# Kernel tuning notes

Hardware: AMD Instinct MI355X
Metric: run time of the kernel (lower is better)

The kernel has to match this reference:

```python
import jax, jax.numpy as jnp
import numpy as np

B, L, D = 4, 2048, 1024
H = 16
HD = D // H  # head_dim = 64
BASE = 10000.0


def rope_cos_sin(seq_len, head_dim, dtype=jnp.float32):
    inv_freq = 1.0 / (BASE ** (jnp.arange(0, head_dim, 2, dtype=jnp.float32) / head_dim))
    t = jnp.arange(seq_len, dtype=jnp.float32)
    freqs = jnp.outer(t, inv_freq)  # [L, HD/2]
    return jnp.cos(freqs).astype(dtype), jnp.sin(freqs).astype(dtype)


def apply_rope(x, cos, sin):
    # x: [B, H, L, HD]; cos/sin: [L, HD/2]
    x1 = x[..., ::2]
    x2 = x[..., 1::2]
    c = cos[None, None, :, :]
    s = sin[None, None, :, :]
    # NOTE: original concatenates halves (does not re-interleave)
    return jnp.concatenate([x1 * c - x2 * s, x1 * s + x2 * c], axis=-1)


def setup_inputs() -> dict:
    key = jax.random.key(0)
    k1, k2, k3 = jax.random.split(key, 3)
    x = jax.random.normal(k1, (B, L, D), dtype=jnp.float32)
    W_qkv = jax.random.normal(k2, (3 * D, D), dtype=jnp.float32) * (D ** -0.5)
    W_proj = jax.random.normal(k3, (D, D), dtype=jnp.float32) * (D ** -0.5)
    return {"x": x, "W_qkv": W_qkv, "W_proj": W_proj}


def reference(x, W_qkv, W_proj):
    b, l, d = x.shape
    scale = HD ** -0.5
    qkv = jnp.einsum('bld,ed->ble', x, W_qkv)            # [B, L, 3D]
    qkv = qkv.reshape(b, l, 3, H, HD)
    q, k, v = (jnp.transpose(qkv[:, :, i], (0, 2, 1, 3)) for i in range(3))  # [B,H,L,HD]
    cos, sin = rope_cos_sin(l, HD, x.dtype)
    q = apply_rope(q, cos, sin)
    k = apply_rope(k, cos, sin)
    attn = jnp.einsum('bhqd,bhkd->bhqk', q, k) * scale   # [B,H,L,L]
    attn = jax.nn.softmax(attn, axis=-1)
    out = jnp.einsum('bhqk,bhkd->bhqd', attn, v)         # [B,H,L,HD]
    out = jnp.transpose(out, (0, 2, 1, 3)).reshape(b, l, d)
    return jnp.einsum('bld,ed->ble', out, W_proj)
```

## Files before the change

kernel.cpp:

```cpp
#include <hip/hip_runtime.h>
#include <hip/hip_bf16.h>

typedef unsigned short u16;
typedef unsigned int u32;
typedef __attribute__((ext_vector_type(8))) short bf16x8;
typedef __attribute__((ext_vector_type(4))) float f32x4;

#define NL 2048
#define NH 16

__device__ __forceinline__ float bf2f(u16 v) {
    union { float f; unsigned u; } x; x.u = ((unsigned)v) << 16; return x.f;
}
__device__ __forceinline__ u16 f2bf(float f) {
    union { __hip_bfloat16 h; u16 u; } x; x.h = __float2bfloat16(f); return x.u;
}
__device__ __forceinline__ u32 pk2(float a, float b) {
    union { float f; u32 u; } x, y; x.f = a; y.f = b;
    return ((x.u + 0x8000u) >> 16) | ((y.u + 0x8000u) & 0xffff0000u);
}
__device__ __forceinline__ u32 pkt(float lo, float hi) {
    union { float f; u32 u; } x, y; x.f = lo; y.f = hi;
    return __builtin_amdgcn_perm(y.u, x.u, 0x07060302u);
}
#if __has_builtin(__builtin_amdgcn_exp2f)
#define EXP2F(x) __builtin_amdgcn_exp2f(x)
#else
#define EXP2F(x) __expf((x) * 0.69314718056f)
#endif

__device__ __forceinline__ void gload_lds16(const u16* g, u16* l) {
    __builtin_amdgcn_global_load_lds(
        (__attribute__((address_space(1))) void*)(g),
        (__attribute__((address_space(3))) void*)(l), 16, 0, 0);
}

__global__ __launch_bounds__(256) void cast_all_k(const float* __restrict__ x,
                                                  const float* __restrict__ wq,
                                                  const float* __restrict__ wp,
                                                  u16* __restrict__ xo,
                                                  u16* __restrict__ wqo,
                                                  u16* __restrict__ wpo) {
    int i = blockIdx.x * 256 + threadIdx.x;
    const float* src; u16* dst; int off;
    if (i < 2097152)      { src = x;  dst = xo;  off = i; }
    else if (i < 2883584) { src = wq; dst = wqo; off = i - 2097152; }
    else                  { src = wp; dst = wpo; off = i - 2883584; }
    float4 v = *(const float4*)&src[(size_t)off * 4];
    u16 tmp[4] = {f2bf(v.x), f2bf(v.y), f2bf(v.z), f2bf(v.w)};
    *(ushort4*)&dst[(size_t)off * 4] = *(ushort4*)tmp;
}

__global__ __launch_bounds__(256) void rope_table_k(float* __restrict__ cosT,
                                                    float* __restrict__ sinT) {
    int idx = blockIdx.x * 256 + threadIdx.x;
    int l = idx >> 5, i = idx & 31;
    float invf = exp2f(-(float)i * 0.41524101186092029f);
    float ang = (float)l * invf;
    cosT[idx] = cosf(ang);
    sinT[idx] = sinf(ang);
}

template <typename OutT>
__global__ __launch_bounds__(256) void gemm_bt(const u16* __restrict__ A,
                                               const u16* __restrict__ Bm,
                                               OutT* __restrict__ C,
                                               int M, int N, int K) {
    __shared__ u16 As[128][64];
    __shared__ u16 Bs[128][64];
    const int t = threadIdx.x;
    const int lane = t & 63, wave = t >> 6;
    const int quad = lane >> 4, lrow = lane & 15;
    const int wr = wave >> 1, wc = wave & 1;
    const size_t m0 = (size_t)blockIdx.y * 128, n0 = (size_t)blockIdx.x * 128;

    const int srow = wave * 32 + (lane >> 3);
    const int scg  = (lane & 7) ^ (lane >> 3);

    f32x4 acc[4][4];
#pragma unroll
    for (int i = 0; i < 4; ++i)
#pragma unroll
        for (int j = 0; j < 4; ++j) acc[i][j] = (f32x4)0.0f;

    for (int k0 = 0; k0 < K; k0 += 64) {
#pragma unroll
        for (int j = 0; j < 4; ++j) {
            gload_lds16(&A[(m0 + srow + j * 8) * K + k0 + scg * 8],
                        &As[wave * 32 + j * 8][0]);
            gload_lds16(&Bm[(n0 + srow + j * 8) * K + k0 + scg * 8],
                        &Bs[wave * 32 + j * 8][0]);
        }
        __syncthreads();
#pragma unroll
        for (int ks = 0; ks < 2; ++ks) {
            bf16x8 av[4], bv[4];
#pragma unroll
            for (int i = 0; i < 4; ++i)
                av[i] = *(const bf16x8*)
                    &As[wr * 64 + i * 16 + lrow][(((ks << 2) | quad) ^ (lrow & 7)) << 3];
#pragma unroll
            for (int j = 0; j < 4; ++j)
                bv[j] = *(const bf16x8*)
                    &Bs[wc * 64 + j * 16 + lrow][(((ks << 2) | quad) ^ (lrow & 7)) << 3];
#pragma unroll
            for (int i = 0; i < 4; ++i)
#pragma unroll
                for (int j = 0; j < 4; ++j)
                    acc[i][j] = __builtin_amdgcn_mfma_f32_16x16x32_bf16(
                        av[i], bv[j], acc[i][j], 0, 0, 0);
        }
        __syncthreads();
    }
#pragma unroll
    for (int i = 0; i < 4; ++i)
#pragma unroll
        for (int r = 0; r < 4; ++r) {
            size_t row = m0 + wr * 64 + i * 16 + quad * 4 + r;
#pragma unroll
            for (int j = 0; j < 4; ++j) {
                size_t col = n0 + wc * 64 + j * 16 + lrow;
                if constexpr (sizeof(OutT) == 4)
                    C[row * N + col] = acc[i][j][r];
                else
                    C[row * N + col] = f2bf(acc[i][j][r]);
            }
        }
}

__global__ __launch_bounds__(256) void rope_vt_k(const u16* __restrict__ qkv,
                                                 const float* __restrict__ cosT,
                                                 const float* __restrict__ sinT,
                                                 u16* __restrict__ Q,
                                                 u16* __restrict__ Ko,
                                                 u16* __restrict__ VT) {
    __shared__ u16 vtile[64][72];
    const int lt = blockIdx.x, bh = blockIdx.y;
    const int b = bh >> 4, h = bh & 15;
    const int l0 = lt * 64;
    const int t = threadIdx.x;
    const float SC = 0.180336879f;
#pragma unroll
    for (int c = 0; c < 2; ++c) {
        int flat8 = c * 256 + t;
        int li = flat8 >> 3, dg = flat8 & 7;
        const u16* rowp = qkv + (size_t)(b * NL + l0 + li) * 3072 + h * 64 + dg * 8;
        uint4 qv = *(const uint4*)rowp;
        uint4 kv = *(const uint4*)(rowp + 1024);
        uint4 vv = *(const uint4*)(rowp + 2048);
        *(uint4*)&vtile[li][dg * 8] = vv;
        float4 cs = *(const float4*)&cosT[(l0 + li) * 32 + dg * 4];
        float4 sn = *(const float4*)&sinT[(l0 + li) * 32 + dg * 4];
        union { float f; u32 u; } w;
        float e0, o0, e1, o1, e2, o2, e3, o3;
        w.u = qv.x << 16; e0 = w.f; w.u = qv.x & 0xffff0000u; o0 = w.f;
        w.u = qv.y << 16; e1 = w.f; w.u = qv.y & 0xffff0000u; o1 = w.f;
        w.u = qv.z << 16; e2 = w.f; w.u = qv.z & 0xffff0000u; o2 = w.f;
        w.u = qv.w << 16; e3 = w.f; w.u = qv.w & 0xffff0000u; o3 = w.f;
        float c0 = cs.x * SC, c1 = cs.y * SC, c2 = cs.z * SC, c3 = cs.w * SC;
        float s0 = sn.x * SC, s1 = sn.y * SC, s2 = sn.z * SC, s3 = sn.w * SC;
        size_t ob = ((size_t)(b * NH + h) * NL + l0 + li) * 64;
        *(uint2*)&Q[ob + dg * 4] =
            make_uint2(pk2(e0 * c0 - o0 * s0, e1 * c1 - o1 * s1),
                       pk2(e2 * c2 - o2 * s2, e3 * c3 - o3 * s3));
        *(uint2*)&Q[ob + 32 + dg * 4] =
            make_uint2(pk2(e0 * s0 + o0 * c0, e1 * s1 + o1 * c1),
                       pk2(e2 * s2 + o2 * c2, e3 * s3 + o3 * c3));
        float f0, g0, f1, g1, f2, g2, f3, g3;
        w.u = kv.x << 16; f0 = w.f; w.u = kv.x & 0xffff0000u; g0 = w.f;
        w.u = kv.y << 16; f1 = w.f; w.u = kv.y & 0xffff0000u; g1 = w.f;
        w.u = kv.z << 16; f2 = w.f; w.u = kv.z & 0xffff0000u; g2 = w.f;
        w.u = kv.w << 16; f3 = w.f; w.u = kv.w & 0xffff0000u; g3 = w.f;
        *(uint2*)&Ko[ob + dg * 4] =
            make_uint2(pk2(f0 * cs.x - g0 * sn.x, f1 * cs.y - g1 * sn.y),
                       pk2(f2 * cs.z - g2 * sn.z, f3 * cs.w - g3 * sn.w));
        *(uint2*)&Ko[ob + 32 + dg * 4] =
            make_uint2(pk2(f0 * sn.x + g0 * cs.x, f1 * sn.y + g1 * cs.y),
                       pk2(f2 * sn.z + g2 * cs.z, f3 * sn.w + g3 * cs.w));
    }
    __syncthreads();
#pragma unroll
    for (int c = 0; c < 2; ++c) {
        int flat8 = c * 256 + t;
        int d = flat8 >> 3, lg = flat8 & 7;
        u16 tmp[8];
#pragma unroll
        for (int e = 0; e < 8; ++e) tmp[e] = vtile[lg * 8 + e][d];
        *(uint4*)&VT[((size_t)(bh * 64 + d)) * NL + l0 + lg * 8] = *(uint4*)tmp;
    }
}

__global__ __launch_bounds__(512, 4) void attn_k(const u16* __restrict__ Q,
                                                 const u16* __restrict__ Kg,
                                                 const u16* __restrict__ VT,
                                                 u16* __restrict__ Og) {
    __shared__ __align__(16) char smem[65536];
    u16 (*KsB)[64][64] = (u16(*)[64][64])(smem);
    u16 (*VsB)[64][64] = (u16(*)[64][64])(smem + 16384);
    u16* PsBase = (u16*)(smem + 32768);
    const int t = threadIdx.x;
    const int lane = t & 63, wave = t >> 6;
    const int quad = lane >> 4, lq = lane & 15;
    u16* PsW = PsBase + wave * 2048;

    const int qt = blockIdx.x, bh = blockIdx.y;
    const int q0 = qt * 256;
    const size_t qkbase = (size_t)bh * NL * 64;

    const int rsub = lane >> 3;
    const int scg  = (lane & 7) ^ rsub;

    u16 (*Qtmp)[64] = (u16(*)[64])(smem + 32768);
#pragma unroll
    for (int j = 0; j < 4; ++j)
        gload_lds16(&Q[qkbase + (size_t)(q0 + wave * 32 + j * 8 + rsub) * 64 + scg * 8],
                    &Qtmp[wave * 32 + j * 8][0]);
    const u16* kptr = Kg + qkbase + (size_t)(wave * 8 + rsub) * 64 + scg * 8;
    const u16* vptr = VT + qkbase + (size_t)(wave * 8 + rsub) * NL + scg * 8;
    gload_lds16(kptr, &KsB[0][wave * 8][0]);
    gload_lds16(vptr, &VsB[0][wave * 8][0]);
    kptr += 64 * 64;
    vptr += 64;
    __syncthreads();
    bf16x8 bq[2][2];
#pragma unroll
    for (int qh = 0; qh < 2; ++qh)
#pragma unroll
        for (int ks = 0; ks < 2; ++ks)
            bq[qh][ks] = *(const bf16x8*)
                &Qtmp[wave * 32 + qh * 16 + lq][(((ks << 2) | quad) ^ (lq & 7)) << 3];

    const bf16x8 ones = (bf16x8)(short)16256;
    f32x4 ot[2][4];
#pragma unroll
    for (int qh = 0; qh < 2; ++qh)
#pragma unroll
        for (int mt = 0; mt < 4; ++mt) ot[qh][mt] = (f32x4)0.0f;
    f32x4 lacc[2] = {(f32x4)0.0f, (f32x4)0.0f};

    for (int kc = 0; kc < NL / 64; ++kc) {
        __syncthreads();
        if (kc < NL / 64 - 1) {
            gload_lds16(kptr, &KsB[(kc + 1) & 1][wave * 8][0]);
            gload_lds16(vptr, &VsB[(kc + 1) & 1][wave * 8][0]);
            kptr += 64 * 64;
            vptr += 64;
        }
        const int cur = kc & 1;

        f32x4 st[2][4];
#pragma unroll
        for (int qh = 0; qh < 2; ++qh)
#pragma unroll
            for (int mt = 0; mt < 4; ++mt) st[qh][mt] = (f32x4)0.0f;
#pragma unroll
        for (int ks = 0; ks < 2; ++ks)
#pragma unroll
            for (int mt = 0; mt < 4; ++mt) {
                bf16x8 ak = *(const bf16x8*)
                    &KsB[cur][mt * 16 + lq][(((ks << 2) | quad) ^ (lq & 7)) << 3];
                st[0][mt] = __builtin_amdgcn_mfma_f32_16x16x32_bf16(ak, bq[0][ks], st[0][mt], 0, 0, 0);
                st[1][mt] = __builtin_amdgcn_mfma_f32_16x16x32_bf16(ak, bq[1][ks], st[1][mt], 0, 0, 0);
            }

#pragma unroll
        for (int qh = 0; qh < 2; ++qh)
#pragma unroll
            for (int mt = 0; mt < 4; ++mt) {
                int pblk = (mt * 2 + (quad >> 1)) ^ (lq & 7);
                *(uint2*)&PsW[(qh * 16 + lq) * 64 + pblk * 8 + (quad & 1) * 4] =
                    make_uint2(pkt(EXP2F(st[qh][mt][0]), EXP2F(st[qh][mt][1])),
                               pkt(EXP2F(st[qh][mt][2]), EXP2F(st[qh][mt][3])));
            }
        __builtin_amdgcn_s_waitcnt(0xc07f);

#pragma unroll
        for (int ks = 0; ks < 2; ++ks) {
            const int sw = (((ks << 2) | quad) ^ (lq & 7)) * 8;
            bf16x8 bp0 = *(const bf16x8*)&PsW[lq * 64 + sw];
            bf16x8 bp1 = *(const bf16x8*)&PsW[(16 + lq) * 64 + sw];
            lacc[0] = __builtin_amdgcn_mfma_f32_16x16x32_bf16(ones, bp0, lacc[0], 0, 0, 0);
            lacc[1] = __builtin_amdgcn_mfma_f32_16x16x32_bf16(ones, bp1, lacc[1], 0, 0, 0);
#pragma unroll
            for (int mt = 0; mt < 4; ++mt) {
                bf16x8 av = *(const bf16x8*)
                    &VsB[cur][mt * 16 + lq][(((ks << 2) | quad) ^ (lq & 7)) << 3];
                ot[0][mt] = __builtin_amdgcn_mfma_f32_16x16x32_bf16(av, bp0, ot[0][mt], 0, 0, 0);
                ot[1][mt] = __builtin_amdgcn_mfma_f32_16x16x32_bf16(av, bp1, ot[1][mt], 0, 0, 0);
            }
        }
    }

    __syncthreads();
    float* OT_ls = (float*)(smem + wave * 4352);
    float* Ls_ls = (float*)(smem + 34816);
    const int b = bh >> 4, h = bh & 15;
    const int qq = lane >> 2, dblk = lane & 3;
#pragma unroll
    for (int qh = 0; qh < 2; ++qh) {
#pragma unroll
        for (int mt = 0; mt < 4; ++mt)
#pragma unroll
            for (int r = 0; r < 4; ++r)
                OT_ls[(mt * 16 + quad * 4 + r) * 17 + lq] = ot[qh][mt][r];
        if (quad == 0) Ls_ls[wave * 16 + lq] = lacc[qh][0];
        __builtin_amdgcn_s_waitcnt(0xc07f);

        float rls = 1.0f / Ls_ls[wave * 16 + qq];
        u16 tmp[16];
#pragma unroll
        for (int e = 0; e < 16; ++e)
            tmp[e] = f2bf(OT_ls[(dblk * 16 + e) * 17 + qq] * rls);
        size_t orow = (size_t)b * NL + q0 + wave * 32 + qh * 16 + qq;
        size_t obase = orow * 1024 + h * 64 + dblk * 16;
        *(uint4*)&Og[obase] = *(uint4*)&tmp[0];
        *(uint4*)&Og[obase + 8] = *(uint4*)&tmp[8];
    }
}

extern "C" void kernel_launch(void* const* d_in, const int* in_sizes, int n_in,
                              void* d_out, int out_size, void* d_ws, size_t ws_size,
                              hipStream_t stream) {
    const float* x     = (const float*)d_in[0];
    const float* Wqkv  = (const float*)d_in[1];
    const float* Wproj = (const float*)d_in[2];
    float* out = (float*)d_out;

    char* ws = (char*)d_ws;
    u16* qkv     = (u16*)ws;
    u16* attnout = (u16*)ws;
    u16* Qw      = (u16*)(ws + 50331648);
    u16* Kw      = (u16*)(ws + 67108864);
    u16* VTw     = (u16*)(ws + 83886080);
    float* cosT  = (float*)(ws + 100663296);
    float* sinT  = (float*)(ws + 100925440);
    u16* x_bf    = (u16*)(ws + 101187584);
    u16* Wqkv_bf = (u16*)(ws + 117964800);
    u16* Wproj_bf= (u16*)(ws + 124256256);

    rope_table_k<<<256, 256, 0, stream>>>(cosT, sinT);
    cast_all_k<<<12288, 256, 0, stream>>>(x, Wqkv, Wproj, x_bf, Wqkv_bf, Wproj_bf);
    gemm_bt<u16><<<dim3(24, 64), 256, 0, stream>>>(x_bf, Wqkv_bf, qkv, 8192, 3072, 1024);
    rope_vt_k<<<dim3(32, 64), 256, 0, stream>>>(qkv, cosT, sinT, Qw, Kw, VTw);
    attn_k<<<dim3(8, 64), 512, 0, stream>>>(Qw, Kw, VTw, attnout);
    gemm_bt<float><<<dim3(8, 64), 256, 0, stream>>>(attnout, Wproj_bf, out, 8192, 1024, 1024);
}
```

Before: 268.6 us.

## Use 256x256-tile pipelined GEMM with 8 waves for QKV projection

Replaces the QKV projection GEMM with a new kernel that uses 256x256 output tiles, 512 threads and double-buffered LDS staging through direct global-to-LDS loads. Each K step is split into four quadrant phases that interleave prefetch, barriers and MFMA bursts, with s_setprio raised around the MFMAs. The larger tile is meant to raise arithmetic intensity and overlap loads with compute, at the cost of 128KB of shared memory per block and a grid of only 384 blocks, which limits occupancy and load balance.

```diff
diff --git a/kernel.cpp b/kernel.cpp
--- a/kernel.cpp
+++ b/kernel.cpp
@@ -126,6 +126,149 @@
                     C[row * N + col] = f2bf(acc[i][j][r]);
             }
         }
+}
+
+__global__ __launch_bounds__(512, 2) void gemm256_bt(const u16* __restrict__ A,
+                                                     const u16* __restrict__ Bm,
+                                                     u16* __restrict__ C,
+                                                     int M, int N, int K) {
+    __shared__ __align__(16) char smem[131072];
+    const int t = threadIdx.x;
+    const int lane = t & 63, w = t >> 6;
+    const int quad = lane >> 4, lq = lane & 15;
+    const int wm = w >> 2, wn = w & 3;
+    const int rsub = lane >> 3;
+    const int scg  = (lane & 7) ^ rsub;
+    const size_t m0 = (size_t)blockIdx.y * 256, n0 = (size_t)blockIdx.x * 256;
+    const int NT = K >> 6;
+
+#define ASB(buf) ((u16(*)[64])(smem + (size_t)(buf) * 65536))
+#define BSB(buf) ((u16(*)[64])(smem + (size_t)(buf) * 65536 + 32768))
+#define STAGE_A(buf, half, kt) { \
+    const size_t kro_ = (size_t)(kt) * 64 + (size_t)(scg * 8); \
+    gload_lds16(&A[(m0 + (half) * 128 + w * 16 + 0 + rsub) * (size_t)K + kro_], \
+                &ASB(buf)[(half) * 128 + w * 16 + 0][0]); \
+    gload_lds16(&A[(m0 + (half) * 128 + w * 16 + 8 + rsub) * (size_t)K + kro_], \
+                &ASB(buf)[(half) * 128 + w * 16 + 8][0]); }
+#define STAGE_B(buf, half, kt) { \
+    const size_t kro_ = (size_t)(kt) * 64 + (size_t)(scg * 8); \
+    gload_lds16(&Bm[(n0 + (half) * 128 + w * 16 + 0 + rsub) * (size_t)K + kro_], \
+                &BSB(buf)[(half) * 128 + w * 16 + 0][0]); \
+    gload_lds16(&Bm[(n0 + (half) * 128 + w * 16 + 8 + rsub) * (size_t)K + kro_], \
+                &BSB(buf)[(half) * 128 + w * 16 + 8][0]); }
+#define RD_A(dst, rowbase) { \
+    _Pragma("unroll") for (int m_ = 0; m_ < 4; ++m_) \
+    _Pragma("unroll") for (int ks_ = 0; ks_ < 2; ++ks_) \
+        dst[m_][ks_] = *(const bf16x8*) \
+            &Ac[(rowbase) + m_ * 16 + lq][(((ks_ << 2) | quad) ^ (lq & 7)) << 3]; }
+#define RD_B(dst, rowbase) { \
+    _Pragma("unroll") for (int n_ = 0; n_ < 2; ++n_) \
+    _Pragma("unroll") for (int ks_ = 0; ks_ < 2; ++ks_) \
+        dst[n_][ks_] = *(const bf16x8*) \
+            &Bc[(rowbase) + n_ * 16 + lq][(((ks_ << 2) | quad) ^ (lq & 7)) << 3]; }
+#define MM(QM, QN, bvv) { \
+    _Pragma("unroll") for (int m_ = 0; m_ < 4; ++m_) \
+    _Pragma("unroll") for (int n_ = 0; n_ < 2; ++n_) \
+    _Pragma("unroll") for (int ks_ = 0; ks_ < 2; ++ks_) \
+        acc[QM][QN][m_][n_] = __builtin_amdgcn_mfma_f32_16x16x32_bf16( \
+            av[m_][ks_], bvv[n_][ks_], acc[QM][QN][m_][n_], 0, 0, 0); }
+
+    f32x4 acc[2][2][4][2];
+#pragma unroll
+    for (int a = 0; a < 2; ++a)
+#pragma unroll
+        for (int b = 0; b < 2; ++b)
+#pragma unroll
+            for (int m = 0; m < 4; ++m)
+#pragma unroll
+                for (int n = 0; n < 2; ++n) acc[a][b][m][n] = (f32x4)0.0f;
+    bf16x8 av[4][2], bv0[2][2], bv1[2][2];
+
+    STAGE_A(0, 0, 0); STAGE_B(0, 0, 0); STAGE_B(0, 1, 0); STAGE_A(0, 1, 0);
+    asm volatile("s_waitcnt vmcnt(4)" ::: "memory");
+    __builtin_amdgcn_s_barrier();
+
+    for (int kt = 0; kt < NT - 1; ++kt) {
+        const int cur = kt & 1, nxt = cur ^ 1;
+        u16 (*Ac)[64] = ASB(cur);
+        u16 (*Bc)[64] = BSB(cur);
+
+        RD_A(av, wm * 64);
+        RD_B(bv0, wn * 32);
+        STAGE_A(nxt, 0, kt + 1);
+        __builtin_amdgcn_s_barrier();
+        __builtin_amdgcn_s_setprio(1);
+        MM(0, 0, bv0);
+        __builtin_amdgcn_s_setprio(0);
+        asm volatile("s_waitcnt vmcnt(4)" ::: "memory");
+        __builtin_amdgcn_s_barrier();
+
+        RD_B(bv1, 128 + wn * 32);
+        STAGE_B(nxt, 0, kt + 1);
+        __builtin_amdgcn_s_barrier();
+        __builtin_amdgcn_s_setprio(1);
+        MM(0, 1, bv1);
+        __builtin_amdgcn_s_setprio(0);
+        asm volatile("s_waitcnt vmcnt(4)" ::: "memory");
+        __builtin_amdgcn_s_barrier();
+
+        RD_A(av, 128 + wm * 64);
+        STAGE_B(nxt, 1, kt + 1);
+        __builtin_amdgcn_s_barrier();
+        __builtin_amdgcn_s_setprio(1);
+        MM(1, 1, bv1);
+        __builtin_amdgcn_s_setprio(0);
+        __builtin_amdgcn_s_barrier();
+
+        RD_B(bv0, wn * 32);
+        STAGE_A(nxt, 1, kt + 1);
+        __builtin_amdgcn_s_barrier();
+        __builtin_amdgcn_s_setprio(1);
+        MM(1, 0, bv0);
+        __builtin_amdgcn_s_setprio(0);
+        asm volatile("s_waitcnt vmcnt(4)" ::: "memory");
+        __builtin_amdgcn_s_barrier();
+    }
+
+    {
+        u16 (*Ac)[64] = ASB((NT - 1) & 1);
+        u16 (*Bc)[64] = BSB((NT - 1) & 1);
+        RD_A(av, wm * 64);
+        RD_B(bv0, wn * 32);
+        MM(0, 0, bv0);
+        asm volatile("s_waitcnt vmcnt(2)" ::: "memory");
+        __builtin_amdgcn_s_barrier();
+        RD_B(bv1, 128 + wn * 32);
+        MM(0, 1, bv1);
+        asm volatile("s_waitcnt vmcnt(0)" ::: "memory");
+        __builtin_amdgcn_s_barrier();
+        RD_A(av, 128 + wm * 64);
+        MM(1, 1, bv1);
+        MM(1, 0, bv0);
+    }
+
+#pragma unroll
+    for (int QM = 0; QM < 2; ++QM)
+#pragma unroll
+        for (int QN = 0; QN < 2; ++QN)
+#pragma unroll
+            for (int m = 0; m < 4; ++m)
+#pragma unroll
+                for (int r = 0; r < 4; ++r) {
+                    size_t row = m0 + QM * 128 + wm * 64 + m * 16 + quad * 4 + r;
+#pragma unroll
+                    for (int n = 0; n < 2; ++n) {
+                        size_t col = n0 + QN * 128 + wn * 32 + n * 16 + lq;
+                        C[row * N + col] = f2bf(acc[QM][QN][m][n][r]);
+                    }
+                }
+#undef ASB
+#undef BSB
+#undef STAGE_A
+#undef STAGE_B
+#undef RD_A
+#undef RD_B
+#undef MM
 }
 
 __global__ __launch_bounds__(256) void rope_vt_k(const u16* __restrict__ qkv,
@@ -340,7 +483,7 @@
 
     rope_table_k<<<256, 256, 0, stream>>>(cosT, sinT);
     cast_all_k<<<12288, 256, 0, stream>>>(x, Wqkv, Wproj, x_bf, Wqkv_bf, Wproj_bf);
-    gemm_bt<u16><<<dim3(24, 64), 256, 0, stream>>>(x_bf, Wqkv_bf, qkv, 8192, 3072, 1024);
+    gemm256_bt<<<dim3(12, 32), 512, 0, stream>>>(x_bf, Wqkv_bf, qkv, 8192, 3072, 1024);
     rope_vt_k<<<dim3(32, 64), 256, 0, stream>>>(qkv, cosT, sinT, Qw, Kw, VTw);
     attn_k<<<dim3(8, 64), 512, 0, stream>>>(Qw, Kw, VTw, attnout);
     gemm_bt<float><<<dim3(8, 64), 256, 0, stream>>>(attnout, Wproj_bf, out, 8192, 1024, 1024);
```

Measured after the change: 265.7 us. No clear change (-1.1%).
